# Performance work log

Measured on AMD Instinct MI355X. Metric: run time of the kernel, lower is better.

Reference implementation:

```python
import jax, jax.numpy as jnp
import numpy as np

B, N, F, A = 8, 2048, 512, 512  # batch, n_dim (tokens), feature_dim, attention_dim
BN_EPS = 1e-5


def setup_inputs() -> dict:
    key = jax.random.key(0)
    ks = jax.random.split(key, 9)
    s_f = 1.0 / np.sqrt(F)
    s_a = 1.0 / np.sqrt(A)
    return {
        "x": jax.random.normal(ks[0], (B, N, F), dtype=jnp.float32),
        "Wq": jax.random.uniform(ks[1], (A, F), jnp.float32, -s_f, s_f),
        "bq": jax.random.uniform(ks[2], (A,), jnp.float32, -s_f, s_f),
        "Wk": jax.random.uniform(ks[3], (A, F), jnp.float32, -s_f, s_f),
        "bk": jax.random.uniform(ks[4], (A,), jnp.float32, -s_f, s_f),
        "Wv": jax.random.uniform(ks[5], (A, F), jnp.float32, -s_f, s_f),
        "bv": jax.random.uniform(ks[6], (A,), jnp.float32, -s_f, s_f),
        "Wo": jax.random.uniform(ks[7], (F, A), jnp.float32, -s_a, s_a),
        "bo": jax.random.uniform(ks[8], (F,), jnp.float32, -s_a, s_a),
        "gamma": jnp.ones((N,), dtype=jnp.float32),
        "beta": jnp.zeros((N,), dtype=jnp.float32),
    }


def reference(x, Wq, bq, Wk, bk, Wv, bv, Wo, bo, gamma, beta):
    # QKV projections: [B,N,F] -> [B,N,A]
    q = jnp.einsum("bnf,af->bna", x, Wq) + bq
    k = jnp.einsum("bnf,af->bna", x, Wk) + bk
    v = jnp.einsum("bnf,af->bna", x, Wv) + bv
    # unscaled single-head attention (no 1/sqrt(d) factor, matches source)
    scores = jnp.einsum("bna,bma->bnm", q, k)          # [B,N,N]
    weights = jax.nn.softmax(scores, axis=-1)
    feature = jnp.einsum("bnm,bma->bna", weights, v)    # [B,N,A]
    # LBR: Linear -> BatchNorm1d(n_dim) over channel dim N -> ReLU
    lin = jnp.einsum("bna,fa->bnf", feature, Wo) + bo   # [B,N,F]
    mean = jnp.mean(lin, axis=(0, 2), keepdims=True)    # stats over batch+last dim
    var = jnp.mean(jnp.square(lin - mean), axis=(0, 2), keepdims=True)  # biased var
    bn = gamma[None, :, None] * (lin - mean) * jax.lax.rsqrt(var + BN_EPS) + beta[None, :, None]
    return jax.nn.relu(bn) + x
```

## Files before the change

kernel.cpp:

```cpp
#include <hip/hip_runtime.h>
#include <hip/hip_fp16.h>
#include <stdint.h>

#define B_   8
#define N_   2048
#define F_   512
#define A_   512
#define MTOT (B_ * N_)

typedef unsigned short u16;
typedef unsigned int   u32;
typedef __attribute__((ext_vector_type(8))) __bf16    bf16x8;
typedef __attribute__((ext_vector_type(8))) _Float16  f16x8;
typedef __attribute__((ext_vector_type(4))) float     f32x4;

__device__ __forceinline__ u16 f2bf(float f) {
    u32 u = __builtin_bit_cast(u32, f);
    u32 r = u + 0x7fffu + ((u >> 16) & 1u);
    return (u16)(r >> 16);
}
__device__ __forceinline__ u16 f2h(float f) {
    _Float16 h = (_Float16)f;
    return __builtin_bit_cast(u16, h);
}

__device__ __forceinline__ void gload_lds16(const u16* g, u16* l) {
    __builtin_amdgcn_global_load_lds(
        (const __attribute__((address_space(1))) u32*)(const u32*)g,
        (__attribute__((address_space(3))) u32*)(u32*)l,
        16, 0, 0);
}

#define VMCNT(n) asm volatile("s_waitcnt vmcnt(" #n ")" ::: "memory")

__device__ __forceinline__ void sync_pre() {
    __builtin_amdgcn_sched_barrier(0);
    __builtin_amdgcn_s_barrier();
    asm volatile("s_waitcnt lgkmcnt(0)" ::: "memory");
    __builtin_amdgcn_sched_barrier(0);
}
__device__ __forceinline__ void sync_post() {
    __builtin_amdgcn_sched_barrier(0);
    __builtin_amdgcn_s_barrier();
}

template <int FMT>
__global__ __launch_bounds__(256) void cvt16(const float* __restrict__ in,
                                             u16* __restrict__ out, int n4) {
    int i = blockIdx.x * 256 + threadIdx.x;
    if (i >= n4) return;
    float4 v = ((const float4*)in)[i];
    u32 a, b;
    if constexpr (FMT == 0) {
        a = (u32)f2bf(v.x) | ((u32)f2bf(v.y) << 16);
        b = (u32)f2bf(v.z) | ((u32)f2bf(v.w) << 16);
    } else {
        a = (u32)f2h(v.x) | ((u32)f2h(v.y) << 16);
        b = (u32)f2h(v.z) | ((u32)f2h(v.w) << 16);
    }
    ((uint2*)out)[i] = make_uint2(a, b);
}

template <int BN, int BIAS_MODE, int OUT_FMT, int IN_FMT>
__global__ __launch_bounds__(512, 2)
void gemm8(const u16* __restrict__ A, int lda, long sA,
           const u16* __restrict__ Bm, int ldb, long sB,
           const float* __restrict__ bias,
           void* __restrict__ Cv, int ldc, long sC, int K, int bdiag)
{
    constexpr int UNITS = (BN == 256) ? 4 : 3;
    constexpr int NF = BN / 64;
    __shared__ alignas(16) u16 lds[2 * UNITS * 8192];

    const int z  = blockIdx.z;
    const int m0 = blockIdx.x * 256;
    const int n0 = blockIdx.y * BN;
    const u16* Ag = A  + (long)z * sA + (long)m0 * lda;
    const u16* Bg = Bm + (long)z * sB + (long)n0 * ldb + (long)(m0 >> 11) * bdiag;

    const int t = threadIdx.x;
    const int lane = t & 63;
    const int wave = t >> 6;
    const int wm = wave >> 2, wn = wave & 3;
    const int frow = lane & 15;
    const int fk8 = (lane >> 4) * 8;

    const int srr = t >> 3;
    const int ses = ((t & 7) * 8) ^ ((srr & 7) << 3);

    auto stageA = [&](int buf, int h, int kt) {
        u16* dst = &lds[(buf * UNITS + h) * 8192 + t * 8];
        const u16* g = Ag + kt * 64 + ses;
        gload_lds16(g + (long)(srr + h * 64) * lda,        dst);
        gload_lds16(g + (long)(srr + 128 + h * 64) * lda,  dst + 4096);
    };
    auto stageB = [&](int buf, int h, int kt) {
        u16* dst = &lds[(buf * UNITS + 2 + h) * 8192 + t * 8];
        const u16* g = Bg + kt * 64 + ses;
        int R0;
        if constexpr (BN == 256) R0 = (srr & 31) + ((srr >> 5) << 6) + h * 32;
        else                     R0 = srr;
        int R1 = R0 + ((BN == 256) ? 128 : 64);
        gload_lds16(g + (long)R0 * ldb, dst);
        gload_lds16(g + (long)R1 * ldb, dst + 4096);
    };
    auto rdA = [&](int buf, int q, int i, int ks) -> uint4 {
        int rr = wm * 64 + i * 16 + frow;
        int e  = (ks * 32 + fk8) ^ ((rr & 7) << 3);
        return *(const uint4*)&lds[(buf * UNITS + q) * 8192 + rr * 64 + e];
    };
    auto rdB = [&](int buf, int p, int j, int ks) -> uint4 {
        int rr = wn * 32 + j * 16 + frow;
        int e  = (ks * 32 + fk8) ^ ((rr & 7) << 3);
        return *(const uint4*)&lds[(buf * UNITS + 2 + p) * 8192 + rr * 64 + e];
    };
    auto MF = [&](uint4 a, uint4 b, f32x4 c) -> f32x4 {
        if constexpr (IN_FMT == 0)
            return __builtin_amdgcn_mfma_f32_16x16x32_bf16(
                __builtin_bit_cast(bf16x8, a), __builtin_bit_cast(bf16x8, b), c, 0, 0, 0);
        else
            return __builtin_amdgcn_mfma_f32_16x16x32_f16(
                __builtin_bit_cast(f16x8, a), __builtin_bit_cast(f16x8, b), c, 0, 0, 0);
    };

    f32x4 acc[8][NF];
#pragma unroll
    for (int i = 0; i < 8; i++)
#pragma unroll
        for (int j = 0; j < NF; j++)
#pragma unroll
            for (int r = 0; r < 4; r++) acc[i][j][r] = 0.f;

    uint4 fa[4][2], fb0[2][2], fb1[2][2];
    const int NT = K >> 6;

    if constexpr (BN == 256) {
        stageA(0, 0, 0); stageB(0, 0, 0); stageB(0, 1, 0); stageA(0, 1, 0);
        VMCNT(4);
    } else {
        stageA(0, 0, 0); stageB(0, 0, 0); stageA(0, 1, 0);
        VMCNT(2);
    }
    __builtin_amdgcn_sched_barrier(0);
    __builtin_amdgcn_s_barrier();

    for (int kt = 0; kt < NT; ++kt) {
        const int buf = kt & 1, nb = buf ^ 1;
        const bool st = (kt + 1 < NT);

        if constexpr (BN == 256) {
#pragma unroll
            for (int i = 0; i < 4; i++) { fa[i][0] = rdA(buf, 0, i, 0); fa[i][1] = rdA(buf, 0, i, 1); }
#pragma unroll
            for (int j = 0; j < 2; j++) { fb0[j][0] = rdB(buf, 0, j, 0); fb0[j][1] = rdB(buf, 0, j, 1); }
            if (st) { stageA(nb, 0, kt + 1); VMCNT(4); } else VMCNT(2);
            sync_pre();
            __builtin_amdgcn_s_setprio(1);
#pragma unroll
            for (int ks = 0; ks < 2; ks++)
#pragma unroll
                for (int i = 0; i < 4; i++)
#pragma unroll
                    for (int j = 0; j < 2; j++)
                        acc[i][j] = MF(fa[i][ks], fb0[j][ks], acc[i][j]);
            __builtin_amdgcn_s_setprio(0);
            sync_post();
#pragma unroll
            for (int j = 0; j < 2; j++) { fb1[j][0] = rdB(buf, 1, j, 0); fb1[j][1] = rdB(buf, 1, j, 1); }
            if (st) { stageB(nb, 0, kt + 1); VMCNT(4); } else VMCNT(0);
            sync_pre();
            __builtin_amdgcn_s_setprio(1);
#pragma unroll
            for (int ks = 0; ks < 2; ks++)
#pragma unroll
                for (int i = 0; i < 4; i++)
#pragma unroll
                    for (int j = 0; j < 2; j++)
                        acc[i][2 + j] = MF(fa[i][ks], fb1[j][ks], acc[i][2 + j]);
            __builtin_amdgcn_s_setprio(0);
            sync_post();
#pragma unroll
            for (int i = 0; i < 4; i++) { fa[i][0] = rdA(buf, 1, i, 0); fa[i][1] = rdA(buf, 1, i, 1); }
            if (st) stageB(nb, 1, kt + 1);
            sync_pre();
            __builtin_amdgcn_s_setprio(1);
#pragma unroll
            for (int ks = 0; ks < 2; ks++)
#pragma unroll
                for (int i = 0; i < 4; i++)
#pragma unroll
                    for (int j = 0; j < 2; j++)
                        acc[4 + i][j] = MF(fa[i][ks], fb0[j][ks], acc[4 + i][j]);
            __builtin_amdgcn_s_setprio(0);
            sync_post();
            if (st) { stageA(nb, 1, kt + 1); VMCNT(4); }
            sync_pre();
            __builtin_amdgcn_s_setprio(1);
#pragma unroll
            for (int ks = 0; ks < 2; ks++)
#pragma unroll
                for (int i = 0; i < 4; i++)
#pragma unroll
                    for (int j = 0; j < 2; j++)
                        acc[4 + i][2 + j] = MF(fa[i][ks], fb1[j][ks], acc[4 + i][2 + j]);
            __builtin_amdgcn_s_setprio(0);
            sync_post();
        } else {
#pragma unroll
            for (int i = 0; i < 4; i++) { fa[i][0] = rdA(buf, 0, i, 0); fa[i][1] = rdA(buf, 0, i, 1); }
#pragma unroll
            for (int j = 0; j < 2; j++) { fb0[j][0] = rdB(buf, 0, j, 0); fb0[j][1] = rdB(buf, 0, j, 1); }
            if (st) { stageA(nb, 0, kt + 1); stageB(nb, 0, kt + 1); VMCNT(4); } else VMCNT(0);
            sync_pre();
            __builtin_amdgcn_s_setprio(1);
#pragma unroll
            for (int ks = 0; ks < 2; ks++)
#pragma unroll
                for (int i = 0; i < 4; i++)
#pragma unroll
                    for (int j = 0; j < 2; j++)
                        acc[i][j] = MF(fa[i][ks], fb0[j][ks], acc[i][j]);
            __builtin_amdgcn_s_setprio(0);
            sync_post();
#pragma unroll
            for (int i = 0; i < 4; i++) { fa[i][0] = rdA(buf, 1, i, 0); fa[i][1] = rdA(buf, 1, i, 1); }
            if (st) { stageA(nb, 1, kt + 1); VMCNT(2); }
            sync_pre();
            __builtin_amdgcn_s_setprio(1);
#pragma unroll
            for (int ks = 0; ks < 2; ks++)
#pragma unroll
                for (int i = 0; i < 4; i++)
#pragma unroll
                    for (int j = 0; j < 2; j++)
                        acc[4 + i][j] = MF(fa[i][ks], fb0[j][ks], acc[4 + i][j]);
            __builtin_amdgcn_s_setprio(0);
            sync_post();
        }
    }

    const int rq = (lane >> 4) * 4;
#pragma unroll
    for (int am = 0; am < 8; am++) {
        const int m = m0 + wm * 128 + (am >> 2) * 64 + (am & 3) * 16 + rq;
#pragma unroll
        for (int an = 0; an < NF; an++) {
            const int n = n0 + wn * (BN / 4) + an * 16 + frow;
            float badd = 0.f;
            if (BIAS_MODE == 1) badd = bias[n];
#pragma unroll
            for (int r = 0; r < 4; r++) {
                float v = acc[am][an][r];
                if (BIAS_MODE == 1) v += badd;
                if (BIAS_MODE == 2) v += bias[m + r];
                long idx = (long)(m + r) * ldc + n + (long)z * sC;
                if constexpr (OUT_FMT == 0)      ((u16*)Cv)[idx] = f2bf(v);
                else if constexpr (OUT_FMT == 1) ((float*)Cv)[idx] = v;
                else                             ((u16*)Cv)[idx] = f2h(v);
            }
        }
    }
}

__global__ __launch_bounds__(256) void softmax_rows(u16* __restrict__ S) {
    __shared__ float red[16];
    const long row = blockIdx.x;
    u16* p = S + row * (long)N_;
    const int t = threadIdx.x;
    const int lane = t & 63, wave = t >> 6;

    uint4 raw = ((const uint4*)p)[t];
    const __half2* hp = (const __half2*)&raw;
    float v[8];
#pragma unroll
    for (int j = 0; j < 4; j++) {
        float2 f = __half22float2(hp[j]);
        v[2 * j]     = f.x;
        v[2 * j + 1] = f.y;
    }
    float mx = v[0];
#pragma unroll
    for (int j = 1; j < 8; j++) mx = fmaxf(mx, v[j]);
#pragma unroll
    for (int o = 32; o; o >>= 1) mx = fmaxf(mx, __shfl_xor(mx, o));
    if (lane == 0) red[wave] = mx;
    __syncthreads();
    mx = fmaxf(fmaxf(red[0], red[1]), fmaxf(red[2], red[3]));

    float s = 0.f;
#pragma unroll
    for (int j = 0; j < 8; j++) { v[j] = __expf(v[j] - mx); s += v[j]; }
#pragma unroll
    for (int o = 32; o; o >>= 1) s += __shfl_xor(s, o);
    if (lane == 0) red[8 + wave] = s;
    __syncthreads();
    s = red[8] + red[9] + red[10] + red[11];
    float inv = 1.f / s;
    u32 w[4];
#pragma unroll
    for (int j = 0; j < 4; j++) {
        u32 lo = f2bf(v[2 * j] * inv);
        u32 hi = f2bf(v[2 * j + 1] * inv);
        w[j] = lo | (hi << 16);
    }
    ((uint4*)p)[t] = make_uint4(w[0], w[1], w[2], w[3]);
}

__global__ __launch_bounds__(256) void bn_stats(const float* __restrict__ lin,
                                                float* __restrict__ stats) {
    __shared__ float red[16];
    const int n = blockIdx.x;
    const int t = threadIdx.x;
    const int lane = t & 63, wave = t >> 6;
    float s = 0.f, s2 = 0.f;
    for (int idx = t; idx < 1024; idx += 256) {
        int b = idx >> 7, f4 = idx & 127;
        float4 x = ((const float4*)(lin + ((long)b * N_ + n) * F_))[f4];
        s  += x.x + x.y + x.z + x.w;
        s2 += x.x * x.x + x.y * x.y + x.z * x.z + x.w * x.w;
    }
#pragma unroll
    for (int o = 32; o; o >>= 1) { s += __shfl_xor(s, o); s2 += __shfl_xor(s2, o); }
    if (lane == 0) { red[wave] = s; red[8 + wave] = s2; }
    __syncthreads();
    if (t == 0) {
        float S1 = red[0] + red[1] + red[2] + red[3];
        float S2 = red[8] + red[9] + red[10] + red[11];
        float mean = S1 / 4096.f;
        float var  = S2 / 4096.f - mean * mean;
        stats[n]      = mean;
        stats[N_ + n] = rsqrtf(var + 1e-5f);
    }
}

__global__ __launch_bounds__(256)
void bn_relu_add(const float* __restrict__ lin, const float* __restrict__ x,
                 const float* __restrict__ gamma, const float* __restrict__ beta,
                 const float* __restrict__ stats, float* __restrict__ out) {
    long i4 = (long)blockIdx.x * 256 + threadIdx.x;
    int n = (int)((i4 >> 7) & (N_ - 1));
    float mean = stats[n], rstd = stats[N_ + n];
    float scale = gamma[n] * rstd;
    float shift = beta[n] - mean * scale;
    float4 l  = ((const float4*)lin)[i4];
    float4 xx = ((const float4*)x)[i4];
    float4 o;
    o.x = fmaxf(l.x * scale + shift, 0.f) + xx.x;
    o.y = fmaxf(l.y * scale + shift, 0.f) + xx.y;
    o.z = fmaxf(l.z * scale + shift, 0.f) + xx.z;
    o.w = fmaxf(l.w * scale + shift, 0.f) + xx.w;
    ((float4*)out)[i4] = o;
}

extern "C" void kernel_launch(void* const* d_in, const int* in_sizes, int n_in,
                              void* d_out, int out_size, void* d_ws, size_t ws_size,
                              hipStream_t stream)
{
    (void)in_sizes; (void)n_in; (void)out_size; (void)ws_size;
    const float* x     = (const float*)d_in[0];
    const float* Wq    = (const float*)d_in[1];
    const float* bq    = (const float*)d_in[2];
    const float* Wk    = (const float*)d_in[3];
    const float* bk    = (const float*)d_in[4];
    const float* Wv    = (const float*)d_in[5];
    const float* bv    = (const float*)d_in[6];
    const float* Wo    = (const float*)d_in[7];
    const float* bo    = (const float*)d_in[8];
    const float* gamma = (const float*)d_in[9];
    const float* beta  = (const float*)d_in[10];
    float* out = (float*)d_out;
    char*  ws  = (char*)d_ws;

    const size_t MB = 1024 * 1024;
    u16*   wqkh  = (u16*)(ws + 0);
    u16*   wvh   = (u16*)(ws + 1 * MB);
    u16*   wob   = (u16*)(ws + 1 * MB + 512 * 1024);
    float* stats = (float*)(ws + 2 * MB);
    float* bqk   = (float*)(ws + 2 * MB + 64 * 1024);
    u16*   xh    = (u16*)(ws + 4 * MB);
    u16*   qkh   = (u16*)(ws + 20 * MB);
    u16*   vt    = (u16*)(ws + 52 * MB);
    u16*   S     = (u16*)(ws + 68 * MB);
    u16*   feat  = (u16*)(ws + 132 * MB);
    float* lin   = (float*)(ws + 148 * MB);

    hipMemcpyAsync(bqk,       bq, 512 * sizeof(float), hipMemcpyDeviceToDevice, stream);
    hipMemcpyAsync(bqk + 512, bk, 512 * sizeof(float), hipMemcpyDeviceToDevice, stream);

    cvt16<1><<<8192, 256, 0, stream>>>(x,  xh,  2097152);
    cvt16<1><<<256,  256, 0, stream>>>(Wq, wqkh,          65536);
    cvt16<1><<<256,  256, 0, stream>>>(Wk, wqkh + 262144, 65536);
    cvt16<1><<<256,  256, 0, stream>>>(Wv, wvh, 65536);
    cvt16<0><<<256,  256, 0, stream>>>(Wo, wob, 65536);

    gemm8<256, 1, 2, 1><<<dim3(64, 4, 1), 512, 0, stream>>>(
        xh, 512, 0, wqkh, 512, 0, bqk, qkh, 1024, 0, 512, 0);
    gemm8<128, 2, 0, 1><<<dim3(2, 128, 1), 512, 0, stream>>>(
        wvh, 512, 0, xh, 512, 0, bv, vt, MTOT, 0, 512, 0);
    gemm8<256, 0, 2, 1><<<dim3(8, 8, 8), 512, 0, stream>>>(
        qkh, 1024, (long)N_ * 1024, qkh + 512, 1024, (long)N_ * 1024,
        nullptr, S, N_, (long)N_ * N_, 512, 0);
    softmax_rows<<<MTOT, 256, 0, stream>>>(S);
    gemm8<128, 0, 0, 0><<<dim3(64, 4, 1), 512, 0, stream>>>(
        S, N_, 0, vt, MTOT, 0, nullptr, feat, A_, 0, 2048, 2048);
    gemm8<128, 1, 1, 0><<<dim3(64, 4, 1), 512, 0, stream>>>(
        feat, 512, 0, wob, 512, 0, bo, lin, 512, 0, 512, 0);

    bn_stats<<<2048, 256, 0, stream>>>(lin, stats);
    bn_relu_add<<<8192, 256, 0, stream>>>(lin, x, gamma, beta, stats, out);
}
```

Measured before the change: 214.2 us.

## Fuse softmax row sums into QK GEMM, exp into PV GEMM, BN stats into output GEMM

Removes the separate softmax pass over the fp16 score matrix. The QK GEMM epilogue now accumulates per-row exp sums with atomics, and a new PV kernel applies exp(s - log rowsum) while staging S tiles into LDS. BN statistics (sum and sum of squares) are also accumulated with atomics in the final GEMM epilogue, which drops the bn_stats kernel. The softmax skips max subtraction and relies on the unscaled scores staying in fp16/fp32 exp range, so overflow is a risk. The fused paths add atomic traffic and extra register-staged A loads in the PV GEMM.

New measurement: 250.4 us. 1.17x slower.

```diff
diff --git a/kernel.cpp b/kernel.cpp
--- a/kernel.cpp
+++ b/kernel.cpp
@@ -23,6 +23,9 @@
     _Float16 h = (_Float16)f;
     return __builtin_bit_cast(u16, h);
 }
+__device__ __forceinline__ float hrt(float f) {
+    return (float)(_Float16)f;
+}
 
 __device__ __forceinline__ void gload_lds16(const u16* g, u16* l) {
     __builtin_amdgcn_global_load_lds(
@@ -32,15 +35,17 @@
 }
 
 #define VMCNT(n) asm volatile("s_waitcnt vmcnt(" #n ")" ::: "memory")
+#define LGKM0()  asm volatile("s_waitcnt lgkmcnt(0)" ::: "memory")
+#define SCHEDB() __builtin_amdgcn_sched_barrier(0)
 
 __device__ __forceinline__ void sync_pre() {
-    __builtin_amdgcn_sched_barrier(0);
+    SCHEDB();
     __builtin_amdgcn_s_barrier();
-    asm volatile("s_waitcnt lgkmcnt(0)" ::: "memory");
-    __builtin_amdgcn_sched_barrier(0);
+    LGKM0();
+    SCHEDB();
 }
 __device__ __forceinline__ void sync_post() {
-    __builtin_amdgcn_sched_barrier(0);
+    SCHEDB();
     __builtin_amdgcn_s_barrier();
 }
 
@@ -61,19 +66,22 @@
     ((uint2*)out)[i] = make_uint2(a, b);
 }
 
-template <int BN, int BIAS_MODE, int OUT_FMT, int IN_FMT>
+template <int BN, int BIAS_MODE, int OUT_FMT, int IN_FMT, int EPI, int XS>
 __global__ __launch_bounds__(512, 2)
 void gemm8(const u16* __restrict__ A, int lda, long sA,
            const u16* __restrict__ Bm, int ldb, long sB,
            const float* __restrict__ bias,
-           void* __restrict__ Cv, int ldc, long sC, int K, int bdiag)
+           void* __restrict__ Cv, int ldc, long sC, int K, int bdiag,
+           float* __restrict__ aux)
 {
     constexpr int UNITS = (BN == 256) ? 4 : 3;
     constexpr int NF = BN / 64;
     __shared__ alignas(16) u16 lds[2 * UNITS * 8192];
 
-    const int z  = blockIdx.z;
-    const int m0 = blockIdx.x * 256;
+    int bx = blockIdx.x, bz = blockIdx.z;
+    if constexpr (XS == 1) { int tt = bx; bx = bz; bz = tt; }
+    const int z  = bz;
+    const int m0 = bx * 256;
     const int n0 = blockIdx.y * BN;
     const u16* Ag = A  + (long)z * sA + (long)m0 * lda;
     const u16* Bg = Bm + (long)z * sB + (long)n0 * ldb + (long)(m0 >> 11) * bdiag;
@@ -141,7 +149,7 @@
         stageA(0, 0, 0); stageB(0, 0, 0); stageA(0, 1, 0);
         VMCNT(2);
     }
-    __builtin_amdgcn_sched_barrier(0);
+    SCHEDB();
     __builtin_amdgcn_s_barrier();
 
     for (int kt = 0; kt < NT; ++kt) {
@@ -244,92 +252,198 @@
     for (int am = 0; am < 8; am++) {
         const int m = m0 + wm * 128 + (am >> 2) * 64 + (am & 3) * 16 + rq;
 #pragma unroll
-        for (int an = 0; an < NF; an++) {
-            const int n = n0 + wn * (BN / 4) + an * 16 + frow;
-            float badd = 0.f;
-            if (BIAS_MODE == 1) badd = bias[n];
-#pragma unroll
-            for (int r = 0; r < 4; r++) {
+        for (int r = 0; r < 4; r++) {
+            float vs[NF];
+#pragma unroll
+            for (int an = 0; an < NF; an++) {
+                const int n = n0 + wn * (BN / 4) + an * 16 + frow;
                 float v = acc[am][an][r];
-                if (BIAS_MODE == 1) v += badd;
+                if (BIAS_MODE == 1) v += bias[n];
                 if (BIAS_MODE == 2) v += bias[m + r];
+                vs[an] = v;
                 long idx = (long)(m + r) * ldc + n + (long)z * sC;
                 if constexpr (OUT_FMT == 0)      ((u16*)Cv)[idx] = f2bf(v);
                 else if constexpr (OUT_FMT == 1) ((float*)Cv)[idx] = v;
                 else                             ((u16*)Cv)[idx] = f2h(v);
             }
+            if constexpr (EPI == 1) {
+                float se = 0.f;
+#pragma unroll
+                for (int an = 0; an < NF; an++) se += __expf(hrt(vs[an]));
+#pragma unroll
+                for (int o = 1; o < 16; o <<= 1) se += __shfl_xor(se, o);
+                if (frow == 0)
+                    atomicAdd(&aux[(long)z * N_ + m + r], se);
+            }
+            if constexpr (EPI == 2) {
+                float s1 = 0.f, s2 = 0.f;
+#pragma unroll
+                for (int an = 0; an < NF; an++) { s1 += vs[an]; s2 += vs[an] * vs[an]; }
+#pragma unroll
+                for (int o = 1; o < 16; o <<= 1) { s1 += __shfl_xor(s1, o); s2 += __shfl_xor(s2, o); }
+                if (frow == 0) {
+                    int tok = (m + r) & (N_ - 1);
+                    atomicAdd(&aux[tok], s1);
+                    atomicAdd(&aux[N_ + tok], s2);
+                }
+            }
         }
     }
 }
 
-__global__ __launch_bounds__(256) void softmax_rows(u16* __restrict__ S) {
-    __shared__ float red[16];
-    const long row = blockIdx.x;
-    u16* p = S + row * (long)N_;
+__global__ __launch_bounds__(512, 2)
+void pv8(const u16* __restrict__ S, const u16* __restrict__ vt,
+         const float* __restrict__ rowsum, u16* __restrict__ C)
+{
+    constexpr int UNITS = 3;
+    __shared__ alignas(16) u16 lds[2 * UNITS * 8192];
+
+    const int bx = blockIdx.x;
+    const int mt = ((bx & 7) << 3) | (bx >> 3);
+    const int m0 = mt * 256;
+    const int n0 = blockIdx.y * 128;
+    const int batch = mt >> 3;
+    const u16* Ag = S  + (long)m0 * N_;
+    const u16* Bg = vt + (long)n0 * MTOT + batch * N_;
+
     const int t = threadIdx.x;
-    const int lane = t & 63, wave = t >> 6;
-
-    uint4 raw = ((const uint4*)p)[t];
-    const __half2* hp = (const __half2*)&raw;
-    float v[8];
-#pragma unroll
-    for (int j = 0; j < 4; j++) {
-        float2 f = __half22float2(hp[j]);
-        v[2 * j]     = f.x;
-        v[2 * j + 1] = f.y;
+    const int lane = t & 63;
+    const int wave = t >> 6;
+    const int wm = wave >> 2, wn = wave & 3;
+    const int frow = lane & 15;
+    const int fk8 = (lane >> 4) * 8;
+
+    const int srr = t >> 3;
+    const int ses = ((t & 7) * 8) ^ ((srr & 7) << 3);
+
+    float ls0 = __logf(rowsum[m0 + srr]);
+    float ls1 = __logf(rowsum[m0 + srr + 64]);
+    float ls2 = __logf(rowsum[m0 + srr + 128]);
+    float ls3 = __logf(rowsum[m0 + srr + 192]);
+
+    uint4 areg[4];
+    auto aload = [&](int kel) {
+        const u16* gp = Ag + kel + ses;
+        areg[0] = *(const uint4*)(gp + (long)(srr      ) * N_);
+        areg[1] = *(const uint4*)(gp + (long)(srr + 128) * N_);
+        areg[2] = *(const uint4*)(gp + (long)(srr +  64) * N_);
+        areg[3] = *(const uint4*)(gp + (long)(srr + 192) * N_);
+    };
+    auto xf8 = [&](uint4 a, float ls) -> uint4 {
+        const __half2* hp = (const __half2*)&a;
+        u32 w[4];
+#pragma unroll
+        for (int j = 0; j < 4; j++) {
+            float2 f = __half22float2(hp[j]);
+            float p0 = __expf(f.x - ls);
+            float p1 = __expf(f.y - ls);
+            w[j] = (u32)f2bf(p0) | ((u32)f2bf(p1) << 16);
+        }
+        return make_uint4(w[0], w[1], w[2], w[3]);
+    };
+    auto wr_xf = [&](int buf) {
+        *(uint4*)&lds[(buf * UNITS + 0) * 8192 + t * 8]        = xf8(areg[0], ls0);
+        *(uint4*)&lds[(buf * UNITS + 0) * 8192 + 4096 + t * 8] = xf8(areg[1], ls2);
+        *(uint4*)&lds[(buf * UNITS + 1) * 8192 + t * 8]        = xf8(areg[2], ls1);
+        *(uint4*)&lds[(buf * UNITS + 1) * 8192 + 4096 + t * 8] = xf8(areg[3], ls3);
+    };
+    auto stageBv = [&](int buf, int kel) {
+        u16* dst = &lds[(buf * UNITS + 2) * 8192 + t * 8];
+        const u16* g = Bg + kel + ses;
+        gload_lds16(g + (long)srr * MTOT, dst);
+        gload_lds16(g + (long)(srr + 64) * MTOT, dst + 4096);
+    };
+    auto rdA = [&](int buf, int q, int i, int ks) -> uint4 {
+        int rr = wm * 64 + i * 16 + frow;
+        int e  = (ks * 32 + fk8) ^ ((rr & 7) << 3);
+        return *(const uint4*)&lds[(buf * UNITS + q) * 8192 + rr * 64 + e];
+    };
+    auto rdB = [&](int buf, int j, int ks) -> uint4 {
+        int rr = wn * 32 + j * 16 + frow;
+        int e  = (ks * 32 + fk8) ^ ((rr & 7) << 3);
+        return *(const uint4*)&lds[(buf * UNITS + 2) * 8192 + rr * 64 + e];
+    };
+
+    f32x4 acc[8][2];
+#pragma unroll
+    for (int i = 0; i < 8; i++)
+#pragma unroll
+        for (int j = 0; j < 2; j++)
+#pragma unroll
+            for (int r = 0; r < 4; r++) acc[i][j][r] = 0.f;
+
+    uint4 fa[4][2], fb[2][2];
+    const int NT = N_ >> 6;
+
+    aload(0);
+    VMCNT(0);
+    wr_xf(0);
+    stageBv(0, 0);
+    aload(64);
+    VMCNT(4);
+    LGKM0();
+    SCHEDB();
+    __builtin_amdgcn_s_barrier();
+
+    for (int kt = 0; kt < NT; ++kt) {
+        const int buf = kt & 1, nb = buf ^ 1;
+        const bool st1 = (kt + 1 < NT), st2 = (kt + 2 < NT);
+
+#pragma unroll
+        for (int i = 0; i < 4; i++) { fa[i][0] = rdA(buf, 0, i, 0); fa[i][1] = rdA(buf, 0, i, 1); }
+#pragma unroll
+        for (int j = 0; j < 2; j++) { fb[j][0] = rdB(buf, j, 0); fb[j][1] = rdB(buf, j, 1); }
+        if (st1) {
+            VMCNT(0);
+            wr_xf(nb);
+            stageBv(nb, (kt + 1) << 6);
+            if (st2) aload((kt + 2) << 6);
+        }
+        LGKM0(); SCHEDB();
+        __builtin_amdgcn_s_setprio(1);
+#pragma unroll
+        for (int ks = 0; ks < 2; ks++)
+#pragma unroll
+            for (int i = 0; i < 4; i++)
+#pragma unroll
+                for (int j = 0; j < 2; j++)
+                    acc[i][j] = __builtin_amdgcn_mfma_f32_16x16x32_bf16(
+                        __builtin_bit_cast(bf16x8, fa[i][ks]),
+                        __builtin_bit_cast(bf16x8, fb[j][ks]), acc[i][j], 0, 0, 0);
+        __builtin_amdgcn_s_setprio(0);
+
+#pragma unroll
+        for (int i = 0; i < 4; i++) { fa[i][0] = rdA(buf, 1, i, 0); fa[i][1] = rdA(buf, 1, i, 1); }
+        if (st1) {
+            if (st2) { VMCNT(4); } else { VMCNT(0); }
+        }
+        LGKM0(); SCHEDB();
+        __builtin_amdgcn_s_setprio(1);
+#pragma unroll
+        for (int ks = 0; ks < 2; ks++)
+#pragma unroll
+            for (int i = 0; i < 4; i++)
+#pragma unroll
+                for (int j = 0; j < 2; j++)
+                    acc[4 + i][j] = __builtin_amdgcn_mfma_f32_16x16x32_bf16(
+                        __builtin_bit_cast(bf16x8, fa[i][ks]),
+                        __builtin_bit_cast(bf16x8, fb[j][ks]), acc[4 + i][j], 0, 0, 0);
+        __builtin_amdgcn_s_setprio(0);
+        SCHEDB();
+        __builtin_amdgcn_s_barrier();
     }
-    float mx = v[0];
-#pragma unroll
-    for (int j = 1; j < 8; j++) mx = fmaxf(mx, v[j]);
-#pragma unroll
-    for (int o = 32; o; o >>= 1) mx = fmaxf(mx, __shfl_xor(mx, o));
-    if (lane == 0) red[wave] = mx;
-    __syncthreads();
-    mx = fmaxf(fmaxf(red[0], red[1]), fmaxf(red[2], red[3]));
-
-    float s = 0.f;
-#pragma unroll
-    for (int j = 0; j < 8; j++) { v[j] = __expf(v[j] - mx); s += v[j]; }
-#pragma unroll
-    for (int o = 32; o; o >>= 1) s += __shfl_xor(s, o);
-    if (lane == 0) red[8 + wave] = s;
-    __syncthreads();
-    s = red[8] + red[9] + red[10] + red[11];
-    float inv = 1.f / s;
-    u32 w[4];
-#pragma unroll
-    for (int j = 0; j < 4; j++) {
-        u32 lo = f2bf(v[2 * j] * inv);
-        u32 hi = f2bf(v[2 * j + 1] * inv);
-        w[j] = lo | (hi << 16);
-    }
-    ((uint4*)p)[t] = make_uint4(w[0], w[1], w[2], w[3]);
-}
-
-__global__ __launch_bounds__(256) void bn_stats(const float* __restrict__ lin,
-                                                float* __restrict__ stats) {
-    __shared__ float red[16];
-    const int n = blockIdx.x;
-    const int t = threadIdx.x;
-    const int lane = t & 63, wave = t >> 6;
-    float s = 0.f, s2 = 0.f;
-    for (int idx = t; idx < 1024; idx += 256) {
-        int b = idx >> 7, f4 = idx & 127;
-        float4 x = ((const float4*)(lin + ((long)b * N_ + n) * F_))[f4];
-        s  += x.x + x.y + x.z + x.w;
-        s2 += x.x * x.x + x.y * x.y + x.z * x.z + x.w * x.w;
-    }
-#pragma unroll
-    for (int o = 32; o; o >>= 1) { s += __shfl_xor(s, o); s2 += __shfl_xor(s2, o); }
-    if (lane == 0) { red[wave] = s; red[8 + wave] = s2; }
-    __syncthreads();
-    if (t == 0) {
-        float S1 = red[0] + red[1] + red[2] + red[3];
-        float S2 = red[8] + red[9] + red[10] + red[11];
-        float mean = S1 / 4096.f;
-        float var  = S2 / 4096.f - mean * mean;
-        stats[n]      = mean;
-        stats[N_ + n] = rsqrtf(var + 1e-5f);
+
+    const int rq = (lane >> 4) * 4;
+#pragma unroll
+    for (int am = 0; am < 8; am++) {
+        const int m = m0 + wm * 128 + (am >> 2) * 64 + (am & 3) * 16 + rq;
+#pragma unroll
+        for (int an = 0; an < 2; an++) {
+            const int n = n0 + wn * 32 + an * 16 + frow;
+#pragma unroll
+            for (int r = 0; r < 4; r++)
+                C[(long)(m + r) * A_ + n] = f2bf(acc[am][an][r]);
+        }
     }
 }
 
@@ -339,7 +453,9 @@
                  const float* __restrict__ stats, float* __restrict__ out) {
     long i4 = (long)blockIdx.x * 256 + threadIdx.x;
     int n = (int)((i4 >> 7) & (N_ - 1));
-    float mean = stats[n], rstd = stats[N_ + n];
+    float mean = stats[n] * (1.f / 4096.f);
+    float var  = stats[N_ + n] * (1.f / 4096.f) - mean * mean;
+    float rstd = rsqrtf(var + 1e-5f);
     float scale = gamma[n] * rstd;
     float shift = beta[n] - mean * scale;
     float4 l  = ((const float4*)lin)[i4];
@@ -376,7 +492,8 @@
     u16*   wvh   = (u16*)(ws + 1 * MB);
     u16*   wob   = (u16*)(ws + 1 * MB + 512 * 1024);
     float* stats = (float*)(ws + 2 * MB);
-    float* bqk   = (float*)(ws + 2 * MB + 64 * 1024);
+    float* rowsum= (float*)(ws + 2 * MB + 16 * 1024);
+    float* bqk   = (float*)(ws + 2 * MB + 80 * 1024);
     u16*   xh    = (u16*)(ws + 4 * MB);
     u16*   qkh   = (u16*)(ws + 20 * MB);
     u16*   vt    = (u16*)(ws + 52 * MB);
@@ -384,6 +501,7 @@
     u16*   feat  = (u16*)(ws + 132 * MB);
     float* lin   = (float*)(ws + 148 * MB);
 
+    hipMemsetAsync(stats, 0, 80 * 1024, stream);
     hipMemcpyAsync(bqk,       bq, 512 * sizeof(float), hipMemcpyDeviceToDevice, stream);
     hipMemcpyAsync(bqk + 512, bk, 512 * sizeof(float), hipMemcpyDeviceToDevice, stream);
 
@@ -393,19 +511,16 @@
     cvt16<1><<<256,  256, 0, stream>>>(Wv, wvh, 65536);
     cvt16<0><<<256,  256, 0, stream>>>(Wo, wob, 65536);
 
-    gemm8<256, 1, 2, 1><<<dim3(64, 4, 1), 512, 0, stream>>>(
-        xh, 512, 0, wqkh, 512, 0, bqk, qkh, 1024, 0, 512, 0);
-    gemm8<128, 2, 0, 1><<<dim3(2, 128, 1), 512, 0, stream>>>(
-        wvh, 512, 0, xh, 512, 0, bv, vt, MTOT, 0, 512, 0);
-    gemm8<256, 0, 2, 1><<<dim3(8, 8, 8), 512, 0, stream>>>(
+    gemm8<256, 1, 2, 1, 0, 0><<<dim3(64, 4, 1), 512, 0, stream>>>(
+        xh, 512, 0, wqkh, 512, 0, bqk, qkh, 1024, 0, 512, 0, nullptr);
+    gemm8<128, 2, 0, 1, 0, 0><<<dim3(2, 128, 1), 512, 0, stream>>>(
+        wvh, 512, 0, xh, 512, 0, bv, vt, MTOT, 0, 512, 0, nullptr);
+    gemm8<256, 0, 2, 1, 1, 1><<<dim3(8, 8, 8), 512, 0, stream>>>(
         qkh, 1024, (long)N_ * 1024, qkh + 512, 1024, (long)N_ * 1024,
-        nullptr, S, N_, (long)N_ * N_, 512, 0);
-    softmax_rows<<<MTOT, 256, 0, stream>>>(S);
-    gemm8<128, 0, 0, 0><<<dim3(64, 4, 1), 512, 0, stream>>>(
-        S, N_, 0, vt, MTOT, 0, nullptr, feat, A_, 0, 2048, 2048);
-    gemm8<128, 1, 1, 0><<<dim3(64, 4, 1), 512, 0, stream>>>(
-        feat, 512, 0, wob, 512, 0, bo, lin, 512, 0, 512, 0);
-
-    bn_stats<<<2048, 256, 0, stream>>>(lin, stats);
+        nullptr, S, N_, (long)N_ * N_, 512, 0, rowsum);
+    pv8<<<dim3(64, 4, 1), 512, 0, stream>>>(S, vt, rowsum, feat);
+    gemm8<128, 1, 1, 0, 2, 0><<<dim3(64, 4, 1), 512, 0, stream>>>(
+        feat, 512, 0, wob, 512, 0, bo, lin, 512, 0, 512, 0, stats);
+
     bn_relu_add<<<8192, 256, 0, stream>>>(lin, x, gamma, beta, stats, out);
 }
```
